# Kernel tuning notes

Measured on AMD Instinct MI355X. Metric: run time of the kernel, lower is better.

Reference implementation:

```python
import jax, jax.numpy as jnp
import numpy as np

N = 100000
E = 1600000
F_IN = 128
HID = 128
OUT = 256


def setup_inputs() -> dict:
    key = jax.random.key(0)
    ks = jax.random.split(key, 8)
    node_features = jax.random.normal(ks[0], (N, F_IN), dtype=jnp.float32)
    edge_index = jax.random.randint(ks[1], (2, E), 0, N, dtype=jnp.int64)
    s = 0.05
    W1 = jax.random.normal(ks[2], (F_IN, HID), dtype=jnp.float32) * s
    b1 = jnp.zeros((HID,), dtype=jnp.float32)
    W2 = jax.random.normal(ks[3], (HID, HID), dtype=jnp.float32) * s
    b2 = jnp.zeros((HID,), dtype=jnp.float32)
    # note: source's Linear(hidden_dim, output_dim) is inconsistent with the
    # 2*hidden concat of mean+max pool; we size fc as [2*HID, OUT] so it runs.
    fcW = jax.random.normal(ks[4], (2 * HID, OUT), dtype=jnp.float32) * s
    fcb = jnp.zeros((OUT,), dtype=jnp.float32)
    return {"node_features": node_features, "edge_index": edge_index,
            "W1": W1, "b1": b1, "W2": W2, "b2": b2, "fcW": fcW, "fcb": fcb}


def _gcn_norm(edge_index, num_nodes):
    # add self loops, compute symmetric normalization (PyG GCNConv default)
    loops = jnp.arange(num_nodes, dtype=edge_index.dtype)
    src = jnp.concatenate([edge_index[0], loops])
    dst = jnp.concatenate([edge_index[1], loops])
    ones = jnp.ones(src.shape[0], dtype=jnp.float32)
    deg = jax.ops.segment_sum(ones, dst, num_segments=num_nodes)  # [N]
    dinv = jnp.where(deg > 0, jax.lax.rsqrt(deg), 0.0)
    norm = dinv[src] * dinv[dst]  # [E+N]
    return src, dst, norm


def _gcn_conv(x, W, b, src, dst, norm, num_nodes):
    h = x @ W                                     # [N, H] dense transform
    msg = h[src] * norm[:, None]                  # gather + per-edge scale
    out = jax.ops.segment_sum(msg, dst, num_segments=num_nodes)  # scatter-add
    return out + b


def reference(node_features, edge_index, W1, b1, W2, b2, fcW, fcb):
    num_nodes = node_features.shape[0]
    src, dst, norm = _gcn_norm(edge_index, num_nodes)
    x = jax.nn.relu(_gcn_conv(node_features, W1, b1, src, dst, norm, num_nodes))
    x = jax.nn.relu(_gcn_conv(x, W2, b2, src, dst, norm, num_nodes))
    # batch vector is all zeros -> single graph: global mean + max pool
    pooled = jnp.concatenate([jnp.mean(x, axis=0, keepdims=True),
                              jnp.max(x, axis=0, keepdims=True)], axis=1)  # [1, 2H]
    # dropout is identity at inference
    return pooled @ fcW + fcb  # [1, OUT]
```

## Files before the change

### kernel.cpp

```cpp
#include <hip/hip_runtime.h>
#include <hip/hip_bf16.h>
#include <hip/hip_fp16.h>

static constexpr int FDIM = 128;
static constexpr int NBKT = 1024;
static constexpr int BHB = 128;

typedef _Float16 h8 __attribute__((ext_vector_type(8)));
typedef _Float16 h2 __attribute__((ext_vector_type(2)));
typedef float v4f __attribute__((ext_vector_type(4)));


__global__ __launch_bounds__(256) void k_prep(const int* __restrict__ dst,
                                              int* __restrict__ bucketPart,
                                              const float* __restrict__ W1,
                                              const float* __restrict__ W2,
                                              _Float16* __restrict__ T1,
                                              _Float16* __restrict__ T2,
                                              float* __restrict__ colsum,
                                              float* __restrict__ colmax, int ne) {
    const int b = blockIdx.x;
    if (b < BHB) {
        __shared__ int lb[NBKT];
        for (int j = threadIdx.x; j < NBKT; j += 256) lb[j] = 0;
        __syncthreads();
        const int stride = BHB * 256;
        for (int e = b * 256 + threadIdx.x; e < ne; e += stride)
            atomicAdd(&lb[dst[e] >> 7], 1);
        __syncthreads();
        int* mine = bucketPart + b * NBKT;
        for (int j = threadIdx.x; j < NBKT; j += 256) mine[j] = lb[j];
    } else if (b < BHB + 128) {
        int bb = b - BHB;
        const float* W = (bb < 64) ? W1 : W2;
        _Float16* T = (bb < 64) ? T1 : T2;
        int idx = (bb & 63) * 256 + threadIdx.x;
        int k = idx >> 7, nn = idx & 127;
        T[nn * FDIM + k] = (_Float16)W[idx];
    } else {
        int i = threadIdx.x;
        if (i < FDIM) { colsum[i] = 0.0f; colmax[i] = 0.0f; }
    }
}

__global__ __launch_bounds__(1024) void k_scanB(const int* __restrict__ bucketPart,
                                                int* __restrict__ bucketBase,
                                                int* __restrict__ bucketCur) {
    __shared__ int tmp[NBKT];
    int t = threadIdx.x;
    int v = 0;
    for (int k = 0; k < BHB; k++) v += bucketPart[k * NBKT + t];
    tmp[t] = v;
    __syncthreads();
    for (int off = 1; off < NBKT; off <<= 1) {
        int u = (t >= off) ? tmp[t - off] : 0;
        __syncthreads();
        tmp[t] += u;
        __syncthreads();
    }
    int excl = tmp[t] - v;
    bucketBase[t] = excl;
    bucketCur[t] = excl;
}

__global__ __launch_bounds__(256) void k_binfill(const int* __restrict__ src,
                                                 const int* __restrict__ dst,
                                                 int* __restrict__ bucketCur,
                                                 unsigned long long* __restrict__ ebuf,
                                                 int ne) {
    __shared__ int lcnt[NBKT];
    __shared__ int lbase[NBKT];
    const int e0 = blockIdx.x * 8192;
    for (int j = threadIdx.x; j < NBKT; j += 256) lcnt[j] = 0;
    __syncthreads();

    int dcache[32];
#pragma unroll
    for (int i = 0; i < 32; i++) {
        int e = e0 + i * 256 + threadIdx.x;
        int d = (e < ne) ? dst[e] : -1;
        dcache[i] = d;
        if (d >= 0) atomicAdd(&lcnt[d >> 7], 1);
    }
    __syncthreads();

    for (int j = threadIdx.x; j < NBKT; j += 256) {
        int c = lcnt[j];
        lbase[j] = c ? atomicAdd(&bucketCur[j], c) : 0;
        lcnt[j] = 0;
    }
    __syncthreads();

#pragma unroll
    for (int i = 0; i < 32; i++) {
        int e = e0 + i * 256 + threadIdx.x;
        if (e < ne) {
            int d = dcache[i];
            int s = src[e];
            int b = d >> 7;
            int lp = atomicAdd(&lcnt[b], 1);
            ebuf[lbase[b] + lp] =
                ((unsigned long long)(unsigned)d << 32) | (unsigned)s;
        }
    }
}

__global__ __launch_bounds__(256) void k_bucketproc(const unsigned long long* __restrict__ ebuf,
                                                    const int* __restrict__ bucketBase,
                                                    const int* __restrict__ bucketEnd,
                                                    int* __restrict__ work,
                                                    float* __restrict__ dinv,
                                                    int* __restrict__ csr, int n) {
    __shared__ int cnt[128];
    __shared__ int scn[128];
    const int b = blockIdx.x;
    const int base = b << 7;
    const int beg = bucketBase[b], end = bucketEnd[b];

    if (threadIdx.x < 128) cnt[threadIdx.x] = 0;
    __syncthreads();
    for (int i = beg + threadIdx.x; i < end; i += 256) {
        int d = (int)(ebuf[i] >> 32);
        atomicAdd(&cnt[d & 127], 1);
    }
    __syncthreads();

    int v = 0;
    if (threadIdx.x < 128) { v = cnt[threadIdx.x]; scn[threadIdx.x] = v; }
    __syncthreads();
    for (int off = 1; off < 128; off <<= 1) {
        int t = 0;
        if (threadIdx.x < 128 && threadIdx.x >= off) t = scn[threadIdx.x - off];
        __syncthreads();
        if (threadIdx.x < 128) scn[threadIdx.x] += t;
        __syncthreads();
    }
    if (threadIdx.x < 128) {
        int node = base + threadIdx.x;
        if (node < n) {
            int w = beg + scn[threadIdx.x] - v;
            work[node] = w;
            dinv[node] = 1.0f / sqrtf(1.0f + (float)v);
            cnt[threadIdx.x] = w;
        }
    }
    __syncthreads();

    for (int i = beg + threadIdx.x; i < end; i += 256) {
        unsigned long long p = ebuf[i];
        int d = (int)(p >> 32);
        int s = (int)(p & 0xffffffffu);
        int pos = atomicAdd(&cnt[d & 127], 1);
        csr[pos] = s;
    }
}


template <typename T>
__global__ __launch_bounds__(256) void k_gemm_f16(const T* __restrict__ X,
                                                  const _Float16* __restrict__ WT,
                                                  const float* __restrict__ dinv,
                                                  _Float16* __restrict__ H, int n) {
    __shared__ _Float16 sA[FDIM * FDIM];
    __shared__ _Float16 sB[FDIM * FDIM];
    const int t = threadIdx.x;
    const int lane = t & 63;
    const int w = t >> 6;
    const int rowhalf = w >> 1, colhalf = w & 1;

    for (int i = 0; i < 8; i++) {
        int f = i * 256 + t;
        int nn = f >> 4, g = f & 15;
        ((float4*)sB)[nn * 16 + ((g ^ nn) & 15)] = ((const float4*)WT)[f];
    }

    const int ntiles = (n + 127) >> 7;
    for (int tile = blockIdx.x; tile < ntiles; tile += gridDim.x) {
        const int R0 = tile << 7;
        __syncthreads();
        for (int i = 0; i < 8; i++) {
            int f = i * 256 + t;
            int row = f >> 4, g = f & 15;
            int gr = min(R0 + row, n - 1);
            h8 val;
            if constexpr (sizeof(T) == 4) {
                const float4* xp = (const float4*)(X + (size_t)gr * FDIM + g * 8);
                float4 u0 = xp[0], u1 = xp[1];
                val[0] = (_Float16)u0.x; val[1] = (_Float16)u0.y;
                val[2] = (_Float16)u0.z; val[3] = (_Float16)u0.w;
                val[4] = (_Float16)u1.x; val[5] = (_Float16)u1.y;
                val[6] = (_Float16)u1.z; val[7] = (_Float16)u1.w;
            } else {
                val = ((const h8*)(X + (size_t)gr * FDIM))[g];
            }
            ((h8*)sA)[row * 16 + ((g ^ row) & 15)] = val;
        }
        __syncthreads();

        v4f acc[4][4];
#pragma unroll
        for (int rt = 0; rt < 4; rt++)
#pragma unroll
            for (int ct = 0; ct < 4; ct++)
                acc[rt][ct] = (v4f){0.f, 0.f, 0.f, 0.f};

#pragma unroll
        for (int s = 0; s < 4; s++) {
            const int g0 = s * 4 + (lane >> 4);
            h8 af[4], bf[4];
#pragma unroll
            for (int rt = 0; rt < 4; rt++) {
                int row = rowhalf * 64 + rt * 16 + (lane & 15);
                af[rt] = ((const h8*)sA)[row * 16 + ((g0 ^ row) & 15)];
            }
#pragma unroll
            for (int ct = 0; ct < 4; ct++) {
                int nn = colhalf * 64 + ct * 16 + (lane & 15);
                bf[ct] = ((const h8*)sB)[nn * 16 + ((g0 ^ nn) & 15)];
            }
#pragma unroll
            for (int rt = 0; rt < 4; rt++)
#pragma unroll
                for (int ct = 0; ct < 4; ct++)
                    acc[rt][ct] = __builtin_amdgcn_mfma_f32_16x16x32_f16(
                        af[rt], bf[ct], acc[rt][ct], 0, 0, 0);
        }

        const int rb = R0 + rowhalf * 64 + (lane >> 4) * 4;
        const int cb = colhalf * 64 + (lane & 15);
#pragma unroll
        for (int rt = 0; rt < 4; rt++)
#pragma unroll
            for (int reg = 0; reg < 4; reg++) {
                int grow = rb + rt * 16 + reg;
                if (grow < n) {
                    float d = dinv[grow];
                    _Float16* hp = H + (size_t)grow * FDIM + cb;
#pragma unroll
                    for (int ct = 0; ct < 4; ct++)
                        hp[ct * 16] = (_Float16)(acc[rt][ct][reg] * d);
                }
            }
    }
}


__global__ __launch_bounds__(256) void k_aggregate(const int* __restrict__ work,
                                                   const int* __restrict__ csr,
                                                   const float* __restrict__ dinv,
                                                   const _Float16* __restrict__ hs,
                                                   const float* __restrict__ bias,
                                                   _Float16* __restrict__ out,
                                                   int n, int ne) {
    const int lane = threadIdx.x & 63;
    const int nwaves = gridDim.x * 4;
    int wid = (blockIdx.x * 256 + threadIdx.x) >> 6;
    const h2* hs2 = (const h2*)hs;
    const float2 bb = ((const float2*)bias)[lane];

    for (int node = wid; node < n; node += nwaves) {
        int beg = work[node];
        int end = (node + 1 < n) ? work[node + 1] : ne;
        float dd = dinv[node];
        h2 hv = hs2[(size_t)node * 64 + lane];
        float ax = (float)hv[0];
        float ay = (float)hv[1];
        for (int chunk = beg; chunk < end; chunk += 64) {
            int m = end - chunk; if (m > 64) m = 64;
            int myidx = (lane < m) ? csr[chunk + lane] : 0;
            int j = 0;
            for (; j + 8 <= m; j += 8) {
                int s0 = __shfl(myidx, j + 0);
                int s1 = __shfl(myidx, j + 1);
                int s2 = __shfl(myidx, j + 2);
                int s3 = __shfl(myidx, j + 3);
                int s4 = __shfl(myidx, j + 4);
                int s5 = __shfl(myidx, j + 5);
                int s6 = __shfl(myidx, j + 6);
                int s7 = __shfl(myidx, j + 7);
                h2 v0 = hs2[(size_t)s0 * 64 + lane];
                h2 v1 = hs2[(size_t)s1 * 64 + lane];
                h2 v2 = hs2[(size_t)s2 * 64 + lane];
                h2 v3 = hs2[(size_t)s3 * 64 + lane];
                h2 v4 = hs2[(size_t)s4 * 64 + lane];
                h2 v5 = hs2[(size_t)s5 * 64 + lane];
                h2 v6 = hs2[(size_t)s6 * 64 + lane];
                h2 v7 = hs2[(size_t)s7 * 64 + lane];
                ax += (float)v0[0] + (float)v1[0] + (float)v2[0] + (float)v3[0]
                    + (float)v4[0] + (float)v5[0] + (float)v6[0] + (float)v7[0];
                ay += (float)v0[1] + (float)v1[1] + (float)v2[1] + (float)v3[1]
                    + (float)v4[1] + (float)v5[1] + (float)v6[1] + (float)v7[1];
            }
            for (; j < m; j++) {
                int s = __shfl(myidx, j);
                h2 v = hs2[(size_t)s * 64 + lane];
                ax += (float)v[0];
                ay += (float)v[1];
            }
        }
        float ox = fmaxf(ax * dd + bb.x, 0.f);
        float oy = fmaxf(ay * dd + bb.y, 0.f);
        h2 o; o[0] = (_Float16)ox; o[1] = (_Float16)oy;
        ((h2*)out)[(size_t)node * 64 + lane] = o;
    }
}


__global__ __launch_bounds__(256) void k_pool_h(const _Float16* __restrict__ X,
                                                float* __restrict__ colsum,
                                                float* __restrict__ colmax, int n) {
    __shared__ float ls[256], lm[256];
    int c = threadIdx.x & 127;
    int grp = threadIdx.x >> 7;
    float s = 0.f, m = 0.f;
    for (int r = blockIdx.x * 2 + grp; r < n; r += gridDim.x * 2) {
        float v = (float)X[(size_t)r * FDIM + c];
        s += v;
        m = fmaxf(m, v);
    }
    ls[threadIdx.x] = s;
    lm[threadIdx.x] = m;
    __syncthreads();
    if (threadIdx.x < 128) {
        s = ls[threadIdx.x] + ls[threadIdx.x + 128];
        m = fmaxf(lm[threadIdx.x], lm[threadIdx.x + 128]);
        unsafeAtomicAdd(&colsum[c], s);
        atomicMax((int*)colmax + c, __float_as_int(m));
    }
}

__global__ __launch_bounds__(256) void k_pool_f(const float* __restrict__ X,
                                                float* __restrict__ colsum,
                                                float* __restrict__ colmax, int n) {
    __shared__ float ls[256], lm[256];
    int c = threadIdx.x & 127;
    int grp = threadIdx.x >> 7;
    float s = 0.f, m = 0.f;
    for (int r = blockIdx.x * 2 + grp; r < n; r += gridDim.x * 2) {
        float v = X[(size_t)r * FDIM + c];
        s += v;
        m = fmaxf(m, v);
    }
    ls[threadIdx.x] = s;
    lm[threadIdx.x] = m;
    __syncthreads();
    if (threadIdx.x < 128) {
        s = ls[threadIdx.x] + ls[threadIdx.x + 128];
        m = fmaxf(lm[threadIdx.x], lm[threadIdx.x + 128]);
        unsafeAtomicAdd(&colsum[c], s);
        atomicMax((int*)colmax + c, __float_as_int(m));
    }
}

__global__ __launch_bounds__(256) void k_fc(const float* __restrict__ colsum,
                                            const float* __restrict__ colmax,
                                            const float* __restrict__ fcW,
                                            const float* __restrict__ fcb,
                                            float* __restrict__ out, float invN) {
    int o = threadIdx.x;
    float acc = fcb[o];
#pragma unroll 4
    for (int k = 0; k < FDIM; k++)
        acc += colsum[k] * invN * fcW[k * 256 + o];
#pragma unroll 4
    for (int k = 0; k < FDIM; k++)
        acc += colmax[k] * fcW[(FDIM + k) * 256 + o];
    out[o] = acc;
}


__global__ __launch_bounds__(256) void k_initF(float* deg, float* cs, float* cm, int n) {
    int i = blockIdx.x * 256 + threadIdx.x;
    if (i < n) deg[i] = 1.0f;
    if (i < FDIM) { cs[i] = 0.0f; cm[i] = 0.0f; }
}
__global__ __launch_bounds__(256) void k_degreeF(const int* dst, float* deg, int ne) {
    int i = blockIdx.x * 256 + threadIdx.x;
    if (i < ne) unsafeAtomicAdd(&deg[dst[i]], 1.0f);
}
__global__ __launch_bounds__(256) void k_rsqrtF(float* deg, int n) {
    int i = blockIdx.x * 256 + threadIdx.x;
    if (i < n) deg[i] = 1.0f / sqrtf(deg[i]);
}
__global__ __launch_bounds__(256) void k_selfinitF(const float* H, const float* dinv,
                                                   float* acc, int n) {
    int i = blockIdx.x * 256 + threadIdx.x;
    if (i >= n * 32) return;
    int row = i >> 5;
    float s = dinv[row]; s *= s;
    float4 v = ((const float4*)H)[i];
    v.x *= s; v.y *= s; v.z *= s; v.w *= s;
    ((float4*)acc)[i] = v;
}
__global__ __launch_bounds__(256) void k_scatterF(const int* src, const int* dst,
                                                  const float* dinv, const float* H,
                                                  float* acc, int ne) {
    int e = (blockIdx.x * 256 + threadIdx.x) >> 6;
    if (e >= ne) return;
    int lane = threadIdx.x & 63;
    int s = src[e], d = dst[e];
    float w = dinv[s] * dinv[d];
    float2 v = ((const float2*)(H + (size_t)s * FDIM))[lane];
    float* ap = acc + (size_t)d * FDIM + lane * 2;
    unsafeAtomicAdd(ap, v.x * w);
    unsafeAtomicAdd(ap + 1, v.y * w);
}
__global__ __launch_bounds__(256) void k_bias_reluF(float* acc, const float* b, int n) {
    int i = blockIdx.x * 256 + threadIdx.x;
    if (i >= n * 32) return;
    float4 bb = ((const float4*)b)[i & 31];
    float4 v = ((float4*)acc)[i];
    v.x = fmaxf(v.x + bb.x, 0.f);
    v.y = fmaxf(v.y + bb.y, 0.f);
    v.z = fmaxf(v.z + bb.z, 0.f);
    v.w = fmaxf(v.w + bb.w, 0.f);
    ((float4*)acc)[i] = v;
}
__global__ __launch_bounds__(256) void k_gemm128F(const float* X, const float* W,
                                                   float* H, int n) {
    __shared__ float sW[FDIM * FDIM];
    for (int i = threadIdx.x; i < FDIM * FDIM / 4; i += 256)
        ((float4*)sW)[i] = ((const float4*)W)[i];
    __syncthreads();
    const int c = threadIdx.x & 127;
    const int half = threadIdx.x >> 7;
    for (int base = blockIdx.x * 8; base < n; base += gridDim.x * 8) {
        const int r0 = base + half * 4;
        const float* xp0 = X + (size_t)min(r0 + 0, n - 1) * FDIM;
        const float* xp1 = X + (size_t)min(r0 + 1, n - 1) * FDIM;
        const float* xp2 = X + (size_t)min(r0 + 2, n - 1) * FDIM;
        const float* xp3 = X + (size_t)min(r0 + 3, n - 1) * FDIM;
        float a0 = 0.f, a1 = 0.f, a2 = 0.f, a3 = 0.f;
#pragma unroll 8
        for (int k = 0; k < FDIM; k += 4) {
            float w0 = sW[(k + 0) * FDIM + c];
            float w1 = sW[(k + 1) * FDIM + c];
            float w2 = sW[(k + 2) * FDIM + c];
            float w3 = sW[(k + 3) * FDIM + c];
            float4 x0 = *(const float4*)(xp0 + k);
            float4 x1 = *(const float4*)(xp1 + k);
            float4 x2 = *(const float4*)(xp2 + k);
            float4 x3 = *(const float4*)(xp3 + k);
            a0 += x0.x * w0 + x0.y * w1 + x0.z * w2 + x0.w * w3;
            a1 += x1.x * w0 + x1.y * w1 + x1.z * w2 + x1.w * w3;
            a2 += x2.x * w0 + x2.y * w1 + x2.z * w2 + x2.w * w3;
            a3 += x3.x * w0 + x3.y * w1 + x3.z * w2 + x3.w * w3;
        }
        if (r0 + 0 < n) H[(size_t)(r0 + 0) * FDIM + c] = a0;
        if (r0 + 1 < n) H[(size_t)(r0 + 1) * FDIM + c] = a1;
        if (r0 + 2 < n) H[(size_t)(r0 + 2) * FDIM + c] = a2;
        if (r0 + 3 < n) H[(size_t)(r0 + 3) * FDIM + c] = a3;
    }
}


extern "C" void kernel_launch(void* const* d_in, const int* in_sizes, int n_in,
                              void* d_out, int out_size, void* d_ws, size_t ws_size,
                              hipStream_t stream) {
    const float* X   = (const float*)d_in[0];
    const int*   ei  = (const int*)d_in[1];
    const float* W1  = (const float*)d_in[2];
    const float* b1  = (const float*)d_in[3];
    const float* W2  = (const float*)d_in[4];
    const float* b2  = (const float*)d_in[5];
    const float* fcW = (const float*)d_in[6];
    const float* fcb = (const float*)d_in[7];
    float* out = (float*)d_out;

    const int n  = in_sizes[0] / FDIM;
    const int ne = in_sizes[1] / 2;
    const int* src = ei;
    const int* dst = ei + ne;

    const int gN = (n + 255) / 256;
    const int gE = (ne + 255) / 256;
    const int nbkt = (n + 127) >> 7;
    const int gB = (ne + 8191) / 8192;

    size_t need = (size_t)ne * 8 + (size_t)n * FDIM * 2 * 2 + 2 * FDIM * FDIM * 2 +
                  ((size_t)n + 2 * FDIM) * 4 +
                  ((size_t)n + (size_t)(BHB + 2) * NBKT + ne) * 4;

    if (ws_size >= need && nbkt <= NBKT) {
        unsigned long long* ebuf = (unsigned long long*)d_ws;
        _Float16* h    = (_Float16*)(ebuf + ne);
        _Float16* xbuf = h + (size_t)n * FDIM;
        _Float16* w1t  = xbuf + (size_t)n * FDIM;
        _Float16* w2t  = w1t + FDIM * FDIM;
        float* dinv    = (float*)(w2t + FDIM * FDIM);
        float* colsum  = dinv + n;
        float* colmax  = colsum + FDIM;
        int* work      = (int*)(colmax + FDIM);
        int* bucketPart= work + n;
        int* bucketBase= bucketPart + BHB * NBKT;
        int* bucketCur = bucketBase + NBKT;
        int* csr       = bucketCur + NBKT;

        k_prep<<<BHB + 128 + 1, 256, 0, stream>>>(dst, bucketPart, W1, W2,
                                                  w1t, w2t, colsum, colmax, ne);
        k_scanB<<<1, NBKT, 0, stream>>>(bucketPart, bucketBase, bucketCur);
        k_binfill<<<gB, 256, 0, stream>>>(src, dst, bucketCur, ebuf, ne);
        k_bucketproc<<<nbkt, 256, 0, stream>>>(ebuf, bucketBase, bucketCur,
                                               work, dinv, csr, n);

        k_gemm_f16<float><<<512, 256, 0, stream>>>(X, w1t, dinv, h, n);
        k_aggregate<<<2048, 256, 0, stream>>>(work, csr, dinv, h, b1, xbuf, n, ne);
        k_gemm_f16<_Float16><<<512, 256, 0, stream>>>(xbuf, w2t, dinv, h, n);
        k_aggregate<<<2048, 256, 0, stream>>>(work, csr, dinv, h, b2, xbuf, n, ne);

        k_pool_h<<<1024, 256, 0, stream>>>(xbuf, colsum, colmax, n);
        k_fc<<<1, 256, 0, stream>>>(colsum, colmax, fcW, fcb, out, 1.0f / (float)n);
    } else {
        float* h      = (float*)d_ws;
        float* acc    = h + (size_t)n * FDIM;
        float* dinv   = acc + (size_t)n * FDIM;
        float* colsum = dinv + n;
        float* colmax = colsum + FDIM;
        const int gV = (n * 32 + 255) / 256;
        const int gS = (int)(((long long)ne * 64 + 255) / 256);

        k_initF<<<gN, 256, 0, stream>>>(dinv, colsum, colmax, n);
        k_degreeF<<<gE, 256, 0, stream>>>(dst, dinv, ne);
        k_rsqrtF<<<gN, 256, 0, stream>>>(dinv, n);

        k_gemm128F<<<1024, 256, 0, stream>>>(X, W1, h, n);
        k_selfinitF<<<gV, 256, 0, stream>>>(h, dinv, acc, n);
        k_scatterF<<<gS, 256, 0, stream>>>(src, dst, dinv, h, acc, ne);
        k_bias_reluF<<<gV, 256, 0, stream>>>(acc, b1, n);

        k_gemm128F<<<1024, 256, 0, stream>>>(acc, W2, h, n);
        k_selfinitF<<<gV, 256, 0, stream>>>(h, dinv, acc, n);
        k_scatterF<<<gS, 256, 0, stream>>>(src, dst, dinv, h, acc, ne);
        k_bias_reluF<<<gV, 256, 0, stream>>>(acc, b2, n);

        k_pool_f<<<1024, 256, 0, stream>>>(acc, colsum, colmax, n);
        k_fc<<<1, 256, 0, stream>>>(colsum, colmax, fcW, fcb, out, 1.0f / (float)n);
    }
}
```

Measured before the change: 383.7 us.

## Pack edge buffer to 32 bits and gather 16-byte rows in aggregation

The binned edge buffer now stores a 7-bit local destination and a 17-bit source in one 32-bit word instead of a 64-bit pair, halving its write and read traffic during CSR construction. The aggregation kernel splits each wave into four 16-lane groups that each gather a full 128-feature fp16 row with 16-byte loads, handling four edges at once, then reduces the groups with cross-lane shuffles. This cuts per-edge load instructions and shuffle count. The packing assumes node ids fit in 17 bits (n ≤ 131072), and padded lanes issue a redundant load with zero weight.

New measurement: 391.9 us. 1.02x slower.

```diff
diff --git a/kernel.cpp b/kernel.cpp
--- a/kernel.cpp
+++ b/kernel.cpp
@@ -66,7 +66,7 @@
 __global__ __launch_bounds__(256) void k_binfill(const int* __restrict__ src,
                                                  const int* __restrict__ dst,
                                                  int* __restrict__ bucketCur,
-                                                 unsigned long long* __restrict__ ebuf,
+                                                 unsigned int* __restrict__ ebuf,
                                                  int ne) {
     __shared__ int lcnt[NBKT];
     __shared__ int lbase[NBKT];
@@ -99,13 +99,12 @@
             int s = src[e];
             int b = d >> 7;
             int lp = atomicAdd(&lcnt[b], 1);
-            ebuf[lbase[b] + lp] =
-                ((unsigned long long)(unsigned)d << 32) | (unsigned)s;
-        }
-    }
-}
-
-__global__ __launch_bounds__(256) void k_bucketproc(const unsigned long long* __restrict__ ebuf,
+            ebuf[lbase[b] + lp] = ((unsigned)(d & 127) << 17) | (unsigned)s;
+        }
+    }
+}
+
+__global__ __launch_bounds__(256) void k_bucketproc(const unsigned int* __restrict__ ebuf,
                                                     const int* __restrict__ bucketBase,
                                                     const int* __restrict__ bucketEnd,
                                                     int* __restrict__ work,
@@ -119,10 +118,8 @@
 
     if (threadIdx.x < 128) cnt[threadIdx.x] = 0;
     __syncthreads();
-    for (int i = beg + threadIdx.x; i < end; i += 256) {
-        int d = (int)(ebuf[i] >> 32);
-        atomicAdd(&cnt[d & 127], 1);
-    }
+    for (int i = beg + threadIdx.x; i < end; i += 256)
+        atomicAdd(&cnt[ebuf[i] >> 17], 1);
     __syncthreads();
 
     int v = 0;
@@ -147,11 +144,9 @@
     __syncthreads();
 
     for (int i = beg + threadIdx.x; i < end; i += 256) {
-        unsigned long long p = ebuf[i];
-        int d = (int)(p >> 32);
-        int s = (int)(p & 0xffffffffu);
-        int pos = atomicAdd(&cnt[d & 127], 1);
-        csr[pos] = s;
+        unsigned p = ebuf[i];
+        int pos = atomicAdd(&cnt[p >> 17], 1);
+        csr[pos] = (int)(p & 0x1FFFFu);
     }
 }
 
@@ -253,55 +248,57 @@
                                                    _Float16* __restrict__ out,
                                                    int n, int ne) {
     const int lane = threadIdx.x & 63;
+    const int grp = lane >> 4;
+    const int sub = lane & 15;
     const int nwaves = gridDim.x * 4;
     int wid = (blockIdx.x * 256 + threadIdx.x) >> 6;
-    const h2* hs2 = (const h2*)hs;
-    const float2 bb = ((const float2*)bias)[lane];
+    const h8* hs8 = (const h8*)hs;
+
+    float bb[8];
+    {
+        const float4* bp = (const float4*)(bias + sub * 8);
+        float4 b0 = bp[0], b1 = bp[1];
+        bb[0] = b0.x; bb[1] = b0.y; bb[2] = b0.z; bb[3] = b0.w;
+        bb[4] = b1.x; bb[5] = b1.y; bb[6] = b1.z; bb[7] = b1.w;
+    }
 
     for (int node = wid; node < n; node += nwaves) {
         int beg = work[node];
         int end = (node + 1 < n) ? work[node + 1] : ne;
-        float dd = dinv[node];
-        h2 hv = hs2[(size_t)node * 64 + lane];
-        float ax = (float)hv[0];
-        float ay = (float)hv[1];
+        float acc[8];
+        h8 hv = hs8[(size_t)node * 16 + sub];
+#pragma unroll
+        for (int k = 0; k < 8; k++) acc[k] = (grp == 0) ? (float)hv[k] : 0.f;
+
         for (int chunk = beg; chunk < end; chunk += 64) {
             int m = end - chunk; if (m > 64) m = 64;
             int myidx = (lane < m) ? csr[chunk + lane] : 0;
-            int j = 0;
-            for (; j + 8 <= m; j += 8) {
-                int s0 = __shfl(myidx, j + 0);
-                int s1 = __shfl(myidx, j + 1);
-                int s2 = __shfl(myidx, j + 2);
-                int s3 = __shfl(myidx, j + 3);
-                int s4 = __shfl(myidx, j + 4);
-                int s5 = __shfl(myidx, j + 5);
-                int s6 = __shfl(myidx, j + 6);
-                int s7 = __shfl(myidx, j + 7);
-                h2 v0 = hs2[(size_t)s0 * 64 + lane];
-                h2 v1 = hs2[(size_t)s1 * 64 + lane];
-                h2 v2 = hs2[(size_t)s2 * 64 + lane];
-                h2 v3 = hs2[(size_t)s3 * 64 + lane];
-                h2 v4 = hs2[(size_t)s4 * 64 + lane];
-                h2 v5 = hs2[(size_t)s5 * 64 + lane];
-                h2 v6 = hs2[(size_t)s6 * 64 + lane];
-                h2 v7 = hs2[(size_t)s7 * 64 + lane];
-                ax += (float)v0[0] + (float)v1[0] + (float)v2[0] + (float)v3[0]
-                    + (float)v4[0] + (float)v5[0] + (float)v6[0] + (float)v7[0];
-                ay += (float)v0[1] + (float)v1[1] + (float)v2[1] + (float)v3[1]
-                    + (float)v4[1] + (float)v5[1] + (float)v6[1] + (float)v7[1];
+            int nj = (m + 3) >> 2;
+            for (int j = 0; j < nj; j++) {
+                int ei = j * 4 + grp;
+                int s = __shfl(myidx, ei);
+                bool valid = ei < m;
+                s = valid ? s : node;
+                float wgt = valid ? 1.f : 0.f;
+                h8 v = hs8[(size_t)s * 16 + sub];
+#pragma unroll
+                for (int k = 0; k < 8; k++)
+                    acc[k] = fmaf(wgt, (float)v[k], acc[k]);
             }
-            for (; j < m; j++) {
-                int s = __shfl(myidx, j);
-                h2 v = hs2[(size_t)s * 64 + lane];
-                ax += (float)v[0];
-                ay += (float)v[1];
-            }
-        }
-        float ox = fmaxf(ax * dd + bb.x, 0.f);
-        float oy = fmaxf(ay * dd + bb.y, 0.f);
-        h2 o; o[0] = (_Float16)ox; o[1] = (_Float16)oy;
-        ((h2*)out)[(size_t)node * 64 + lane] = o;
+        }
+#pragma unroll
+        for (int k = 0; k < 8; k++) {
+            acc[k] += __shfl_xor(acc[k], 16);
+            acc[k] += __shfl_xor(acc[k], 32);
+        }
+        if (grp == 0) {
+            float dd = dinv[node];
+            h8 o;
+#pragma unroll
+            for (int k = 0; k < 8; k++)
+                o[k] = (_Float16)fmaxf(acc[k] * dd + bb[k], 0.f);
+            ((h8*)out)[(size_t)node * 16 + sub] = o;
+        }
     }
 }
 
@@ -477,12 +474,12 @@
     const int nbkt = (n + 127) >> 7;
     const int gB = (ne + 8191) / 8192;
 
-    size_t need = (size_t)ne * 8 + (size_t)n * FDIM * 2 * 2 + 2 * FDIM * FDIM * 2 +
+    size_t need = (size_t)ne * 4 + (size_t)n * FDIM * 2 * 2 + 2 * FDIM * FDIM * 2 +
                   ((size_t)n + 2 * FDIM) * 4 +
                   ((size_t)n + (size_t)(BHB + 2) * NBKT + ne) * 4;
 
     if (ws_size >= need && nbkt <= NBKT) {
-        unsigned long long* ebuf = (unsigned long long*)d_ws;
+        unsigned int* ebuf = (unsigned int*)d_ws;
         _Float16* h    = (_Float16*)(ebuf + ne);
         _Float16* xbuf = h + (size_t)n * FDIM;
         _Float16* w1t  = xbuf + (size_t)n * FDIM;
```
